# Performance work log

Measured on AMD Instinct MI355X. Metric: run time of the kernel, lower is better.

The kernel has to match this reference:

```python
import jax, jax.numpy as jnp
import numpy as np

DIM = 1024
NUM_HEADS = 16
HEAD_DIM = DIM // NUM_HEADS


def setup_inputs() -> dict:
    key = jax.random.key(0)
    ks = jax.random.split(key, 5)
    B, T = 2, 2048
    x = jax.random.normal(ks[0], (B, T, DIM), dtype=jnp.float32)
    s = 1.0 / np.sqrt(DIM)
    W_qkv = jax.random.normal(ks[1], (DIM, 3 * DIM), dtype=jnp.float32) * s
    b_qkv = jnp.zeros((3 * DIM,), dtype=jnp.float32)
    W_out = jax.random.normal(ks[2], (DIM, DIM), dtype=jnp.float32) * s
    b_out = jnp.zeros((DIM,), dtype=jnp.float32)
    return {"x": x, "W_qkv": W_qkv, "b_qkv": b_qkv, "W_out": W_out, "b_out": b_out}


def reference(x, W_qkv, b_qkv, W_out, b_out):
    B, T, D = x.shape
    H, Hd = NUM_HEADS, HEAD_DIM
    qkv = x @ W_qkv + b_qkv                       # [B,T,3D]
    qkv = qkv.reshape(B, T, 3, H, Hd)
    q = jnp.transpose(qkv[:, :, 0], (0, 2, 1, 3))  # [B,H,T,Hd]
    k = jnp.transpose(qkv[:, :, 1], (0, 2, 1, 3))
    v = jnp.transpose(qkv[:, :, 2], (0, 2, 1, 3))
    att = jnp.einsum('bhqd,bhkd->bhqk', q, k) / np.sqrt(Hd)  # [B,H,T,T]
    causal = jnp.tril(jnp.ones((T, T), dtype=bool))
    att = jnp.where(causal[None, None], att, -jnp.inf)
    att = jax.nn.softmax(att, axis=-1)
    out = jnp.einsum('bhqk,bhkd->bhqd', att, v)   # [B,H,T,Hd]
    out = jnp.transpose(out, (0, 2, 1, 3)).reshape(B, T, D)
    return out @ W_out + b_out
```

## Files before the change

kernel.cpp:

```cpp
#include <hip/hip_runtime.h>
#include <hip/hip_bf16.h>

typedef unsigned short u16;
typedef __attribute__((ext_vector_type(8))) short short8;
typedef __attribute__((ext_vector_type(4))) float f32x4;
typedef __attribute__((ext_vector_type(4))) unsigned short u16x4;

#define LOG2E 1.44269504088896340736f
#define QSCALE_F 0.18033688011112042f


__device__ __forceinline__ void gl_lds16(const void* g, void* l) {
  __builtin_amdgcn_global_load_lds(
      (__attribute__((address_space(1))) void*)g,
      (__attribute__((address_space(3))) void*)l, 16, 0, 0);
}

__device__ __forceinline__ float exp2_fast(float x) {
#if __has_builtin(__builtin_amdgcn_exp2f)
  return __builtin_amdgcn_exp2f(x);
#else
  return exp2f(x);
#endif
}

__device__ __forceinline__ u16 f2bf(float f) {
  union { float f; unsigned int i; } v;
  v.f = f;
  unsigned int r = v.i + 0x7fffu + ((v.i >> 16) & 1u);
  return (u16)(r >> 16);
}

__device__ __forceinline__ unsigned int pack_bf2(float lo, float hi) {
  union { __hip_bfloat162 h2; unsigned int u; } c;
  c.h2 = __float22bfloat162_rn(make_float2(lo, hi));
  return c.u;
}


__global__ __launch_bounds__(256) void prep_kernel(
    const float4* __restrict__ x, u16x4* __restrict__ xb,
    const float* __restrict__ Wqkv, u16* __restrict__ WqkvT,
    const float* __restrict__ Wout, u16* __restrict__ WoutT) {
  __shared__ u16 t[64][65];
  int bid = blockIdx.x, tid = threadIdx.x;
  if (bid < 4096) {
    int i = bid * 256 + tid;
    float4 v = x[i];
    u16x4 o;
    o.x = f2bf(v.x); o.y = f2bf(v.y); o.z = f2bf(v.z); o.w = f2bf(v.w);
    xb[i] = o;
    return;
  }
  const float* W;
  u16* WT;
  int K = 1024, N, bxx, byy;
  if (bid < 4864) {
    int tt = bid - 4096;
    W = Wqkv; WT = WqkvT; N = 3072; bxx = tt % 48; byy = tt / 48;
  } else {
    int tt = bid - 4864;
    W = Wout; WT = WoutT; N = 1024; bxx = tt % 16; byy = tt / 16;
  }
  int r0 = byy * 64, c0 = bxx * 64;
  int tx = tid & 63, ty = tid >> 6;
  for (int r = ty; r < 64; r += 4)
    t[r][tx] = f2bf(W[(size_t)(r0 + r) * N + c0 + tx]);
  __syncthreads();
  for (int r = ty; r < 64; r += 4)
    WT[(size_t)(c0 + r) * K + r0 + tx] = t[tx][r];
}


template <bool OUT_F32, int BM, int BN, bool QSC>
__global__ __launch_bounds__(512, 1) void gemm8_kernel(
    const u16* __restrict__ A, const u16* __restrict__ Bt,
    const float* __restrict__ bias, void* __restrict__ Cout,
    int M, int N, int K) {
  constexpr int MI = BM / 32;
  constexpr int NJ = BN / 64;
  constexpr int CH_A = BM / 8;
  constexpr int CH_B = BN / 8;
  constexpr int PER_W = (CH_A + CH_B) / 8;
  __shared__ u16 LDS[2][(BM + BN) * 64];
  int tid = threadIdx.x;
  int w = tid >> 6, lane = tid & 63, l15 = lane & 15, quad = lane >> 4;
  int bid = blockIdx.y * gridDim.x + blockIdx.x;
  int swz = ((bid & 7) << 5) | (bid >> 3);
  int bx = swz % gridDim.x, by = swz / gridDim.x;
  int m0 = by * BM, n0 = bx * BN;
  int wm = (w & 1) * (BM / 2), wn = (w >> 1) * (BN / 4);

  f32x4 acc[MI][NJ];
#pragma unroll
  for (int i = 0; i < MI; ++i)
#pragma unroll
    for (int j = 0; j < NJ; ++j) {
      f32x4 z = {0.f, 0.f, 0.f, 0.f};
      acc[i][j] = z;
    }

  int r8 = lane >> 3;
  int sw = ((lane & 7) ^ r8) * 8;

  const u16* srcp[PER_W];
  int dsto[PER_W];
#pragma unroll
  for (int i = 0; i < PER_W; ++i) {
    int c = w * PER_W + i;
    if (c < CH_A) {
      srcp[i] = A + (size_t)(m0 + c * 8 + r8) * K + sw;
    } else {
      srcp[i] = Bt + (size_t)(n0 + (c - CH_A) * 8 + r8) * K + sw;
    }
    dsto[i] = c * 512;
  }

  int nt = K >> 6;
#pragma unroll
  for (int i = 0; i < PER_W; ++i) gl_lds16(srcp[i], &LDS[0][dsto[i]]);

  for (int t = 0; t < nt; ++t) {
    asm volatile("s_waitcnt vmcnt(0)" ::: "memory");
    __builtin_amdgcn_s_barrier();
    asm volatile("" ::: "memory");
    int cur = t & 1;
    if (t + 1 < nt) {
      int koff = (t + 1) << 6;
#pragma unroll
      for (int i = 0; i < PER_W; ++i)
        gl_lds16(srcp[i] + koff, &LDS[cur ^ 1][dsto[i]]);
    }
    const u16* As = &LDS[cur][0];
    const u16* Bs = &LDS[cur][CH_A * 512];
#pragma unroll
    for (int kh = 0; kh < 2; ++kh) {
      short8 af[MI], bf[NJ];
#pragma unroll
      for (int i = 0; i < MI; ++i) {
        int R = wm + i * 16 + l15;
        af[i] = *(const short8*)(As + R * 64 +
                                 ((kh * 32 + quad * 8) ^ ((R & 7) * 8)));
      }
#pragma unroll
      for (int j = 0; j < NJ; ++j) {
        int R = wn + j * 16 + l15;
        bf[j] = *(const short8*)(Bs + R * 64 +
                                 ((kh * 32 + quad * 8) ^ ((R & 7) * 8)));
      }
#pragma unroll
      for (int i = 0; i < MI; ++i)
#pragma unroll
        for (int j = 0; j < NJ; ++j)
          acc[i][j] = __builtin_amdgcn_mfma_f32_16x16x32_bf16(af[i], bf[j],
                                                              acc[i][j], 0, 0, 0);
    }
  }

  float bv[NJ];
#pragma unroll
  for (int j = 0; j < NJ; ++j) bv[j] = bias[n0 + wn + j * 16 + l15];
#pragma unroll
  for (int i = 0; i < MI; ++i)
#pragma unroll
    for (int j = 0; j < NJ; ++j) {
      int col = n0 + wn + j * 16 + l15;
      bool doq = QSC && (col < 1024);
#pragma unroll
      for (int r = 0; r < 4; ++r) {
        int row = m0 + wm + i * 16 + quad * 4 + r;
        float val = acc[i][j][r] + bv[j];
        if (doq) val *= QSCALE_F;
        if (OUT_F32)
          ((float*)Cout)[(size_t)row * N + col] = val;
        else
          ((u16*)Cout)[(size_t)row * N + col] = f2bf(val);
      }
    }
}


__global__ __launch_bounds__(512, 2) void flash_kernel(
    const u16* __restrict__ qkv, u16* __restrict__ att) {
  __shared__ unsigned int SH[28672];

  int tid = threadIdx.x;
  int w = tid >> 6, half = w >> 2, wq = w & 3;
  int lane = tid & 63, l15 = lane & 15, quad = lane >> 4;
  int bx = blockIdx.x;
  int p = bx >> 5, bh = bx & 31, b = bh >> 4, h = bh & 15;
  const int qs[2] = {15 - p, p};
  const int kmax0 = 2 * qs[0] + 1, kmax1 = 2 * p + 1;
  const int jmax = 16 - p;

  const u16* base = qkv + (size_t)b * 2048 * 3072 + h * 64;
  const u16* kb = base + 1024;
  const u16* vb = base + 2048;

  int ht = tid & 255;
  const int krow = ht >> 3, h7 = ht & 7;
  const int swk = (h7 ^ (krow & 7)) * 8;

  short8 qf[2][2][2];
#pragma unroll
  for (int t = 0; t < 2; ++t) {
    const u16* qtb = base + (size_t)(qs[t] * 128 + wq * 32 + l15) * 3072;
    qf[t][0][0] = *(const short8*)(qtb + quad * 8);
    qf[t][0][1] = *(const short8*)(qtb + 32 + quad * 8);
    qf[t][1][0] = *(const short8*)(qtb + 16 * 3072 + quad * 8);
    qf[t][1][1] = *(const short8*)(qtb + 16 * 3072 + 32 + quad * 8);
  }

  {
    unsigned int* Ks0 = SH + half * 2048;
    gl_lds16(kb + (size_t)(half * 64 + krow) * 3072 + swk,
             (char*)Ks0 + wq * 1024);
    gl_lds16(kb + (size_t)(half * 64 + 32 + krow) * 3072 + swk,
             (char*)Ks0 + 4096 + wq * 1024);
  }
  uint4 vr0 = *(const uint4*)(vb + (size_t)(half * 64 + 2 * krow) * 3072 + h7 * 8);
  uint4 vr1 = *(const uint4*)(vb + (size_t)(half * 64 + 2 * krow + 1) * 3072 + h7 * 8);

  f32x4 o[2][2][4];
#pragma unroll
  for (int t = 0; t < 2; ++t)
#pragma unroll
    for (int qsub = 0; qsub < 2; ++qsub)
#pragma unroll
      for (int jd = 0; jd < 4; ++jd) {
        f32x4 z = {0.f, 0.f, 0.f, 0.f};
        o[t][qsub][jd] = z;
      }
  float lsum[2][2] = {0.f, 0.f, 0.f, 0.f};

  const int psw = (l15 & 7) << 2;
  unsigned int* Pw = SH + 20480 + w * 1024;

  int b3 = 0;
  for (int j = 0; j < jmax; ++j) {
    int kt = 2 * j + half;
    unsigned int* KsH = SH + b3 * 4096 + half * 2048;
    unsigned int* VtH = SH + 12288 + (j & 1) * 4096 + half * 2048;

    {
      const u16* av = (const u16*)&vr0;
      const u16* bvp = (const u16*)&vr1;
#pragma unroll
      for (int jj = 0; jj < 8; ++jj) {
        int d = h7 * 8 + jj;
        VtH[32 * d + (krow ^ ((jj ^ h7) << 2))] =
            (unsigned int)av[jj] | ((unsigned int)bvp[jj] << 16);
      }
    }

    int nb3 = b3 + 1;
    if (nb3 == 3) nb3 = 0;
    if (j + 1 < jmax) {
      int kn = (kt + 2) * 64;
      unsigned int* Ksn = SH + nb3 * 4096 + half * 2048;
      gl_lds16(kb + (size_t)(kn + krow) * 3072 + swk, (char*)Ksn + wq * 1024);
      gl_lds16(kb + (size_t)(kn + 32 + krow) * 3072 + swk,
               (char*)Ksn + 4096 + wq * 1024);
      vr0 = *(const uint4*)(vb + (size_t)(kn + 2 * krow) * 3072 + h7 * 8);
      vr1 = *(const uint4*)(vb + (size_t)(kn + 2 * krow + 1) * 3072 + h7 * 8);
    }
    b3 = nb3;

    asm volatile("s_waitcnt lgkmcnt(0)" ::: "memory");
    __builtin_amdgcn_s_barrier();
    asm volatile("" ::: "memory");

#pragma unroll
    for (int t = 0; t < 2; ++t) {
      int km = t ? kmax1 : kmax0;
      if (kt > km) continue;
      bool last = (kt == km);
      if (last && wq < 2) continue;
      bool domask = last || ((kt == km - 1) && wq < 2);
      int qloc = ((last ? (wq - 2) : wq) << 5) + l15;

      f32x4 s0[4], s1[4];
#pragma unroll
      for (int jn = 0; jn < 4; ++jn) {
        f32x4 z = {-16.f, -16.f, -16.f, -16.f};
        s0[jn] = z;
        s1[jn] = z;
      }
      __builtin_amdgcn_s_setprio(1);
#pragma unroll
      for (int ss = 0; ss < 2; ++ss) {
        short8 a0 = qf[t][0][ss];
        short8 a1 = qf[t][1][ss];
#pragma unroll
        for (int jn = 0; jn < 4; ++jn) {
          int row = jn * 16 + l15;
          short8 bk = *(const short8*)&KsH[32 * row + ((16 * ss + 4 * quad) ^
                                                       ((row & 7) << 2))];
          s0[jn] = __builtin_amdgcn_mfma_f32_16x16x32_bf16(bk, a0, s0[jn], 0, 0, 0);
          s1[jn] = __builtin_amdgcn_mfma_f32_16x16x32_bf16(bk, a1, s1[jn], 0, 0, 0);
        }
      }
      __builtin_amdgcn_s_setprio(0);

#pragma unroll
      for (int qsub = 0; qsub < 2; ++qsub) {
        int qq = qloc + qsub * 16;
        float pvv[4][4];
        if (domask) {
#pragma unroll
          for (int jn = 0; jn < 4; ++jn) {
            f32x4 sv = qsub ? s1[jn] : s0[jn];
#pragma unroll
            for (int r = 0; r < 4; ++r) {
              float e = exp2_fast(sv[r]);
              if (jn * 16 + quad * 4 + r > qq) e = 0.f;
              pvv[jn][r] = e;
            }
          }
        } else {
#pragma unroll
          for (int jn = 0; jn < 4; ++jn) {
            f32x4 sv = qsub ? s1[jn] : s0[jn];
#pragma unroll
            for (int r = 0; r < 4; ++r)
              pvv[jn][r] = exp2_fast(sv[r]);
          }
        }
        float t0 = (pvv[0][0] + pvv[0][1]) + (pvv[0][2] + pvv[0][3]);
        float t1 = (pvv[1][0] + pvv[1][1]) + (pvv[1][2] + pvv[1][3]);
        float t2 = (pvv[2][0] + pvv[2][1]) + (pvv[2][2] + pvv[2][3]);
        float t3 = (pvv[3][0] + pvv[3][1]) + (pvv[3][2] + pvv[3][3]);
        lsum[t][qsub] += (t0 + t1) + (t2 + t3);
#pragma unroll
        for (int jn = 0; jn < 4; ++jn) {
          uint2 dd = make_uint2(pack_bf2(pvv[jn][0], pvv[jn][1]),
                                pack_bf2(pvv[jn][2], pvv[jn][3]));
          *(uint2*)&Pw[qsub * 512 + 32 * l15 +
                       (((jn << 3) + (quad << 1)) ^ psw)] = dd;
        }
      }

      __builtin_amdgcn_s_setprio(1);
#pragma unroll
      for (int ss = 0; ss < 2; ++ss) {
        short8 pf0 = *(const short8*)&Pw[32 * l15 +
                                         (((ss << 4) + (quad << 2)) ^ psw)];
        short8 pf1 = *(const short8*)&Pw[512 + 32 * l15 +
                                         (((ss << 4) + (quad << 2)) ^ psw)];
#pragma unroll
        for (int jd = 0; jd < 4; ++jd) {
          int vrow = jd * 16 + l15;
          int f = (vrow & 7) ^ ((vrow >> 3) & 7);
          short8 bvv = *(const short8*)&VtH[32 * vrow +
                                            (((ss << 4) + (quad << 2)) ^ (f << 2))];
          o[t][0][jd] =
              __builtin_amdgcn_mfma_f32_16x16x32_bf16(bvv, pf0, o[t][0][jd], 0, 0, 0);
          o[t][1][jd] =
              __builtin_amdgcn_mfma_f32_16x16x32_bf16(bvv, pf1, o[t][1][jd], 0, 0, 0);
        }
      }
      __builtin_amdgcn_s_setprio(0);
    }
  }

  float lf[2][2];
#pragma unroll
  for (int t = 0; t < 2; ++t)
#pragma unroll
    for (int qsub = 0; qsub < 2; ++qsub) {
      float v = lsum[t][qsub];
      v += __shfl_xor(v, 16, 64);
      v += __shfl_xor(v, 32, 64);
      lf[t][qsub] = v;
    }

  float* OM = (float*)SH;
  float* LM = (float*)(SH + 8704);
  __syncthreads();
#pragma unroll
  for (int t = 0; t < 2; ++t) {
    if (half == 0) {
#pragma unroll
      for (int qsub = 0; qsub < 2; ++qsub) {
        int q = wq * 32 + qsub * 16 + l15;
#pragma unroll
        for (int jd = 0; jd < 4; ++jd)
          *(float4*)&OM[q * 68 + jd * 16 + quad * 4] = *(float4*)&o[t][qsub][jd];
        if (quad == 0) LM[q] = lf[t][qsub];
      }
    }
    __syncthreads();
    if (half == 1) {
#pragma unroll
      for (int qsub = 0; qsub < 2; ++qsub) {
        int q = wq * 32 + qsub * 16 + l15;
        float lr = lf[t][qsub] + LM[q];
        float inv = 1.f / lr;
        size_t row = (size_t)b * 2048 + qs[t] * 128 + q;
        u16* orow = att + row * 1024 + h * 64 + quad * 4;
#pragma unroll
        for (int jd = 0; jd < 4; ++jd) {
          float4 pa = *(float4*)&OM[q * 68 + jd * 16 + quad * 4];
          uint2 dd = make_uint2(pack_bf2((o[t][qsub][jd][0] + pa.x) * inv,
                                         (o[t][qsub][jd][1] + pa.y) * inv),
                                pack_bf2((o[t][qsub][jd][2] + pa.z) * inv,
                                         (o[t][qsub][jd][3] + pa.w) * inv));
          *(uint2*)(orow + jd * 16) = dd;
        }
      }
    }
    __syncthreads();
  }
}


extern "C" void kernel_launch(void* const* d_in, const int* in_sizes, int n_in,
                              void* d_out, int out_size, void* d_ws,
                              size_t ws_size, hipStream_t stream) {
  const float* x = (const float*)d_in[0];
  const float* Wqkv = (const float*)d_in[1];
  const float* bqkv = (const float*)d_in[2];
  const float* Wout = (const float*)d_in[3];
  const float* bout = (const float*)d_in[4];
  float* out = (float*)d_out;

  char* ws = (char*)d_ws;
  u16* WqkvT = (u16*)(ws);
  u16* WoutT = (u16*)(ws + 6291456);
  u16* qkv = (u16*)(ws + 8388608);
  u16* attn = (u16*)(ws + 33554432);
  u16* xb = (u16*)(ws + 41943040);

  prep_kernel<<<5120, 256, 0, stream>>>((const float4*)x, (u16x4*)xb, Wqkv,
                                        WqkvT, Wout, WoutT);
  gemm8_kernel<false, 256, 192, true><<<dim3(16, 16), 512, 0, stream>>>(
      xb, WqkvT, bqkv, (void*)qkv, 4096, 3072, 1024);
  flash_kernel<<<256, 512, 0, stream>>>(qkv, attn);
  gemm8_kernel<true, 128, 128, false><<<dim3(8, 32), 512, 0, stream>>>(
      attn, WoutT, bout, (void*)out, 4096, 1024, 1024);
}
```

Baseline: 160.6 us.

## Restructure flash attention into smaller 256-thread blocks with 64-row query chunks

The flash kernel now launches 512 blocks of 256 threads instead of 256 blocks of 512. Each block handles two 64-row query chunks, paired as tile 15-p and tile p, and walks the K/V tiles sequentially for both chunks in one flattened loop. This removes the split of the key range across two half-blocks, along with the cross-half partial-sum merge through shared memory. Shared memory use drops and K buffering goes from triple to double, with a barrier every tile. The trade-off is less intra-block K/V reuse, since each wave does one 16-row query slice per tile, and the K/V tiles are loaded again per 64-row chunk.

```diff
diff --git a/kernel.cpp b/kernel.cpp
--- a/kernel.cpp
+++ b/kernel.cpp
@@ -180,67 +180,65 @@
 }
 
 
-__global__ __launch_bounds__(512, 2) void flash_kernel(
+__global__ __launch_bounds__(256, 2) void flash_kernel(
     const u16* __restrict__ qkv, u16* __restrict__ att) {
-  __shared__ unsigned int SH[28672];
+  __shared__ unsigned int SH[10240];
 
   int tid = threadIdx.x;
-  int w = tid >> 6, half = w >> 2, wq = w & 3;
+  int wq = tid >> 6;
   int lane = tid & 63, l15 = lane & 15, quad = lane >> 4;
-  int bx = blockIdx.x;
-  int p = bx >> 5, bh = bx & 31, b = bh >> 4, h = bh & 15;
-  const int qs[2] = {15 - p, p};
-  const int kmax0 = 2 * qs[0] + 1, kmax1 = 2 * p + 1;
-  const int jmax = 16 - p;
+  int bid = blockIdx.x;
+  int ch = bid >> 8;
+  int c = bid & 255;
+  int p = c >> 5, bh = c & 31, b = bh >> 4, h = bh & 15;
+  const int st0 = 15 - p, st1 = p;
+  const int n0t = 2 * st0 + ch + 1;
+  const int n1t = 2 * st1 + ch + 1;
+  const int ntot = n0t + n1t;
 
   const u16* base = qkv + (size_t)b * 2048 * 3072 + h * 64;
   const u16* kb = base + 1024;
   const u16* vb = base + 2048;
 
-  int ht = tid & 255;
-  const int krow = ht >> 3, h7 = ht & 7;
+  const int krow = tid >> 3, h7 = tid & 7;
   const int swk = (h7 ^ (krow & 7)) * 8;
 
-  short8 qf[2][2][2];
+  short8 qf[2][2];
 #pragma unroll
   for (int t = 0; t < 2; ++t) {
-    const u16* qtb = base + (size_t)(qs[t] * 128 + wq * 32 + l15) * 3072;
-    qf[t][0][0] = *(const short8*)(qtb + quad * 8);
-    qf[t][0][1] = *(const short8*)(qtb + 32 + quad * 8);
-    qf[t][1][0] = *(const short8*)(qtb + 16 * 3072 + quad * 8);
-    qf[t][1][1] = *(const short8*)(qtb + 16 * 3072 + 32 + quad * 8);
-  }
-
-  {
-    unsigned int* Ks0 = SH + half * 2048;
-    gl_lds16(kb + (size_t)(half * 64 + krow) * 3072 + swk,
-             (char*)Ks0 + wq * 1024);
-    gl_lds16(kb + (size_t)(half * 64 + 32 + krow) * 3072 + swk,
-             (char*)Ks0 + 4096 + wq * 1024);
-  }
-  uint4 vr0 = *(const uint4*)(vb + (size_t)(half * 64 + 2 * krow) * 3072 + h7 * 8);
-  uint4 vr1 = *(const uint4*)(vb + (size_t)(half * 64 + 2 * krow + 1) * 3072 + h7 * 8);
-
-  f32x4 o[2][2][4];
+    int stt = t ? st1 : st0;
+    const u16* qtb =
+        base + (size_t)(stt * 128 + ch * 64 + wq * 16 + l15) * 3072;
+    qf[t][0] = *(const short8*)(qtb + quad * 8);
+    qf[t][1] = *(const short8*)(qtb + 32 + quad * 8);
+  }
+
+  gl_lds16(kb + (size_t)krow * 3072 + swk, (char*)SH + wq * 1024);
+  gl_lds16(kb + (size_t)(32 + krow) * 3072 + swk,
+           (char*)SH + 4096 + wq * 1024);
+  uint4 vr0 = *(const uint4*)(vb + (size_t)(2 * krow) * 3072 + h7 * 8);
+  uint4 vr1 = *(const uint4*)(vb + (size_t)(2 * krow + 1) * 3072 + h7 * 8);
+
+  f32x4 o[2][4];
 #pragma unroll
   for (int t = 0; t < 2; ++t)
 #pragma unroll
-    for (int qsub = 0; qsub < 2; ++qsub)
-#pragma unroll
-      for (int jd = 0; jd < 4; ++jd) {
-        f32x4 z = {0.f, 0.f, 0.f, 0.f};
-        o[t][qsub][jd] = z;
-      }
-  float lsum[2][2] = {0.f, 0.f, 0.f, 0.f};
+    for (int jd = 0; jd < 4; ++jd) {
+      f32x4 z = {0.f, 0.f, 0.f, 0.f};
+      o[t][jd] = z;
+    }
+  float lsum[2] = {0.f, 0.f};
 
   const int psw = (l15 & 7) << 2;
-  unsigned int* Pw = SH + 20480 + w * 1024;
-
-  int b3 = 0;
-  for (int j = 0; j < jmax; ++j) {
-    int kt = 2 * j + half;
-    unsigned int* KsH = SH + b3 * 4096 + half * 2048;
-    unsigned int* VtH = SH + 12288 + (j & 1) * 4096 + half * 2048;
+  unsigned int* Pw = SH + 8192 + wq * 512;
+  const int qq = (wq << 4) + l15;
+
+  for (int i = 0; i < ntot; ++i) {
+    int t = (i >= n0t) ? 1 : 0;
+    int kt = t ? i - n0t : i;
+    int kml = t ? (n1t - 1) : (n0t - 1);
+    unsigned int* KsH = SH + (i & 1) * 2048;
+    unsigned int* VtH = SH + 4096 + (i & 1) * 2048;
 
     {
       const u16* av = (const u16*)&vr0;
@@ -252,164 +250,107 @@
             (unsigned int)av[jj] | ((unsigned int)bvp[jj] << 16);
       }
     }
-
-    int nb3 = b3 + 1;
-    if (nb3 == 3) nb3 = 0;
-    if (j + 1 < jmax) {
-      int kn = (kt + 2) * 64;
-      unsigned int* Ksn = SH + nb3 * 4096 + half * 2048;
+    asm volatile("s_waitcnt lgkmcnt(0)" ::: "memory");
+    __builtin_amdgcn_s_barrier();
+    asm volatile("" ::: "memory");
+
+    if (i + 1 < ntot) {
+      int t2 = (i + 1 >= n0t) ? 1 : 0;
+      int kt2 = t2 ? (i + 1 - n0t) : (i + 1);
+      int kn = kt2 * 64;
+      unsigned int* Ksn = SH + ((i + 1) & 1) * 2048;
       gl_lds16(kb + (size_t)(kn + krow) * 3072 + swk, (char*)Ksn + wq * 1024);
       gl_lds16(kb + (size_t)(kn + 32 + krow) * 3072 + swk,
                (char*)Ksn + 4096 + wq * 1024);
       vr0 = *(const uint4*)(vb + (size_t)(kn + 2 * krow) * 3072 + h7 * 8);
       vr1 = *(const uint4*)(vb + (size_t)(kn + 2 * krow + 1) * 3072 + h7 * 8);
     }
-    b3 = nb3;
-
-    asm volatile("s_waitcnt lgkmcnt(0)" ::: "memory");
-    __builtin_amdgcn_s_barrier();
-    asm volatile("" ::: "memory");
-
-#pragma unroll
-    for (int t = 0; t < 2; ++t) {
-      int km = t ? kmax1 : kmax0;
-      if (kt > km) continue;
-      bool last = (kt == km);
-      if (last && wq < 2) continue;
-      bool domask = last || ((kt == km - 1) && wq < 2);
-      int qloc = ((last ? (wq - 2) : wq) << 5) + l15;
-
-      f32x4 s0[4], s1[4];
+
+    bool domask = (kt == kml);
+    f32x4 s[4];
+#pragma unroll
+    for (int jn = 0; jn < 4; ++jn) {
+      f32x4 z = {-16.f, -16.f, -16.f, -16.f};
+      s[jn] = z;
+    }
+    __builtin_amdgcn_s_setprio(1);
+#pragma unroll
+    for (int ss = 0; ss < 2; ++ss) {
+      short8 a = qf[t][ss];
 #pragma unroll
       for (int jn = 0; jn < 4; ++jn) {
-        f32x4 z = {-16.f, -16.f, -16.f, -16.f};
-        s0[jn] = z;
-        s1[jn] = z;
-      }
-      __builtin_amdgcn_s_setprio(1);
-#pragma unroll
-      for (int ss = 0; ss < 2; ++ss) {
-        short8 a0 = qf[t][0][ss];
-        short8 a1 = qf[t][1][ss];
-#pragma unroll
-        for (int jn = 0; jn < 4; ++jn) {
-          int row = jn * 16 + l15;
-          short8 bk = *(const short8*)&KsH[32 * row + ((16 * ss + 4 * quad) ^
-                                                       ((row & 7) << 2))];
-          s0[jn] = __builtin_amdgcn_mfma_f32_16x16x32_bf16(bk, a0, s0[jn], 0, 0, 0);
-          s1[jn] = __builtin_amdgcn_mfma_f32_16x16x32_bf16(bk, a1, s1[jn], 0, 0, 0);
-        }
-      }
-      __builtin_amdgcn_s_setprio(0);
-
-#pragma unroll
-      for (int qsub = 0; qsub < 2; ++qsub) {
-        int qq = qloc + qsub * 16;
-        float pvv[4][4];
-        if (domask) {
-#pragma unroll
-          for (int jn = 0; jn < 4; ++jn) {
-            f32x4 sv = qsub ? s1[jn] : s0[jn];
-#pragma unroll
-            for (int r = 0; r < 4; ++r) {
-              float e = exp2_fast(sv[r]);
-              if (jn * 16 + quad * 4 + r > qq) e = 0.f;
-              pvv[jn][r] = e;
-            }
+        int row = jn * 16 + l15;
+        short8 bk = *(const short8*)&KsH[32 * row + ((16 * ss + 4 * quad) ^
+                                                     ((row & 7) << 2))];
+        s[jn] = __builtin_amdgcn_mfma_f32_16x16x32_bf16(bk, a, s[jn], 0, 0, 0);
+      }
+    }
+    __builtin_amdgcn_s_setprio(0);
+
+    {
+      float pvv[4][4];
+      if (domask) {
+#pragma unroll
+        for (int jn = 0; jn < 4; ++jn)
+#pragma unroll
+          for (int r = 0; r < 4; ++r) {
+            float e = exp2_fast(s[jn][r]);
+            if (jn * 16 + quad * 4 + r > qq) e = 0.f;
+            pvv[jn][r] = e;
           }
-        } else {
-#pragma unroll
-          for (int jn = 0; jn < 4; ++jn) {
-            f32x4 sv = qsub ? s1[jn] : s0[jn];
-#pragma unroll
-            for (int r = 0; r < 4; ++r)
-              pvv[jn][r] = exp2_fast(sv[r]);
-          }
-        }
-        float t0 = (pvv[0][0] + pvv[0][1]) + (pvv[0][2] + pvv[0][3]);
-        float t1 = (pvv[1][0] + pvv[1][1]) + (pvv[1][2] + pvv[1][3]);
-        float t2 = (pvv[2][0] + pvv[2][1]) + (pvv[2][2] + pvv[2][3]);
-        float t3 = (pvv[3][0] + pvv[3][1]) + (pvv[3][2] + pvv[3][3]);
-        lsum[t][qsub] += (t0 + t1) + (t2 + t3);
-#pragma unroll
-        for (int jn = 0; jn < 4; ++jn) {
-          uint2 dd = make_uint2(pack_bf2(pvv[jn][0], pvv[jn][1]),
-                                pack_bf2(pvv[jn][2], pvv[jn][3]));
-          *(uint2*)&Pw[qsub * 512 + 32 * l15 +
-                       (((jn << 3) + (quad << 1)) ^ psw)] = dd;
-        }
-      }
-
-      __builtin_amdgcn_s_setprio(1);
-#pragma unroll
-      for (int ss = 0; ss < 2; ++ss) {
-        short8 pf0 = *(const short8*)&Pw[32 * l15 +
-                                         (((ss << 4) + (quad << 2)) ^ psw)];
-        short8 pf1 = *(const short8*)&Pw[512 + 32 * l15 +
-                                         (((ss << 4) + (quad << 2)) ^ psw)];
-#pragma unroll
-        for (int jd = 0; jd < 4; ++jd) {
-          int vrow = jd * 16 + l15;
-          int f = (vrow & 7) ^ ((vrow >> 3) & 7);
-          short8 bvv = *(const short8*)&VtH[32 * vrow +
-                                            (((ss << 4) + (quad << 2)) ^ (f << 2))];
-          o[t][0][jd] =
-              __builtin_amdgcn_mfma_f32_16x16x32_bf16(bvv, pf0, o[t][0][jd], 0, 0, 0);
-          o[t][1][jd] =
-              __builtin_amdgcn_mfma_f32_16x16x32_bf16(bvv, pf1, o[t][1][jd], 0, 0, 0);
-        }
-      }
-      __builtin_amdgcn_s_setprio(0);
-    }
-  }
-
-  float lf[2][2];
-#pragma unroll
-  for (int t = 0; t < 2; ++t)
-#pragma unroll
-    for (int qsub = 0; qsub < 2; ++qsub) {
-      float v = lsum[t][qsub];
-      v += __shfl_xor(v, 16, 64);
-      v += __shfl_xor(v, 32, 64);
-      lf[t][qsub] = v;
-    }
-
-  float* OM = (float*)SH;
-  float* LM = (float*)(SH + 8704);
-  __syncthreads();
+      } else {
+#pragma unroll
+        for (int jn = 0; jn < 4; ++jn)
+#pragma unroll
+          for (int r = 0; r < 4; ++r)
+            pvv[jn][r] = exp2_fast(s[jn][r]);
+      }
+      float t0 = (pvv[0][0] + pvv[0][1]) + (pvv[0][2] + pvv[0][3]);
+      float t1 = (pvv[1][0] + pvv[1][1]) + (pvv[1][2] + pvv[1][3]);
+      float t2 = (pvv[2][0] + pvv[2][1]) + (pvv[2][2] + pvv[2][3]);
+      float t3 = (pvv[3][0] + pvv[3][1]) + (pvv[3][2] + pvv[3][3]);
+      lsum[t] += (t0 + t1) + (t2 + t3);
+#pragma unroll
+      for (int jn = 0; jn < 4; ++jn) {
+        uint2 dd = make_uint2(pack_bf2(pvv[jn][0], pvv[jn][1]),
+                              pack_bf2(pvv[jn][2], pvv[jn][3]));
+        *(uint2*)&Pw[32 * l15 + (((jn << 3) + (quad << 1)) ^ psw)] = dd;
+      }
+    }
+
+    __builtin_amdgcn_s_setprio(1);
+#pragma unroll
+    for (int ss = 0; ss < 2; ++ss) {
+      short8 pf = *(const short8*)&Pw[32 * l15 +
+                                      (((ss << 4) + (quad << 2)) ^ psw)];
+#pragma unroll
+      for (int jd = 0; jd < 4; ++jd) {
+        int vrow = jd * 16 + l15;
+        int f = (vrow & 7) ^ ((vrow >> 3) & 7);
+        short8 bvv = *(const short8*)&VtH[32 * vrow +
+                                          (((ss << 4) + (quad << 2)) ^ (f << 2))];
+        o[t][jd] =
+            __builtin_amdgcn_mfma_f32_16x16x32_bf16(bvv, pf, o[t][jd], 0, 0, 0);
+      }
+    }
+    __builtin_amdgcn_s_setprio(0);
+  }
+
 #pragma unroll
   for (int t = 0; t < 2; ++t) {
-    if (half == 0) {
-#pragma unroll
-      for (int qsub = 0; qsub < 2; ++qsub) {
-        int q = wq * 32 + qsub * 16 + l15;
-#pragma unroll
-        for (int jd = 0; jd < 4; ++jd)
-          *(float4*)&OM[q * 68 + jd * 16 + quad * 4] = *(float4*)&o[t][qsub][jd];
-        if (quad == 0) LM[q] = lf[t][qsub];
-      }
-    }
-    __syncthreads();
-    if (half == 1) {
-#pragma unroll
-      for (int qsub = 0; qsub < 2; ++qsub) {
-        int q = wq * 32 + qsub * 16 + l15;
-        float lr = lf[t][qsub] + LM[q];
-        float inv = 1.f / lr;
-        size_t row = (size_t)b * 2048 + qs[t] * 128 + q;
-        u16* orow = att + row * 1024 + h * 64 + quad * 4;
-#pragma unroll
-        for (int jd = 0; jd < 4; ++jd) {
-          float4 pa = *(float4*)&OM[q * 68 + jd * 16 + quad * 4];
-          uint2 dd = make_uint2(pack_bf2((o[t][qsub][jd][0] + pa.x) * inv,
-                                         (o[t][qsub][jd][1] + pa.y) * inv),
-                                pack_bf2((o[t][qsub][jd][2] + pa.z) * inv,
-                                         (o[t][qsub][jd][3] + pa.w) * inv));
-          *(uint2*)(orow + jd * 16) = dd;
-        }
-      }
-    }
-    __syncthreads();
+    float v = lsum[t];
+    v += __shfl_xor(v, 16, 64);
+    v += __shfl_xor(v, 32, 64);
+    float inv = 1.f / v;
+    int stt = t ? st1 : st0;
+    size_t row = (size_t)b * 2048 + stt * 128 + ch * 64 + wq * 16 + l15;
+    u16* orow = att + row * 1024 + h * 64 + quad * 4;
+#pragma unroll
+    for (int jd = 0; jd < 4; ++jd) {
+      uint2 dd = make_uint2(pack_bf2(o[t][jd][0] * inv, o[t][jd][1] * inv),
+                            pack_bf2(o[t][jd][2] * inv, o[t][jd][3] * inv));
+      *(uint2*)(orow + jd * 16) = dd;
+    }
   }
 }
 
@@ -435,7 +376,7 @@
                                         WqkvT, Wout, WoutT);
   gemm8_kernel<false, 256, 192, true><<<dim3(16, 16), 512, 0, stream>>>(
       xb, WqkvT, bqkv, (void*)qkv, 4096, 3072, 1024);
-  flash_kernel<<<256, 512, 0, stream>>>(qkv, attn);
+  flash_kernel<<<512, 256, 0, stream>>>(qkv, attn);
   gemm8_kernel<true, 128, 128, false><<<dim3(8, 32), 512, 0, stream>>>(
       attn, WoutT, bout, (void*)out, 4096, 1024, 1024);
 }
```

Measured after the change: 172.2 us. 7.2% more time.
